# Kernel optimization log

Hardware: AMD Instinct MI355X
Metric: run time of the kernel (lower is better)

Reference implementation:

```python
import jax, jax.numpy as jnp
import numpy as np

B, T, E = 1024, 200, 64
NU, NM, NC = 100000, 1000000, 1000
D_LAU_IN = 8 * E      # 512
D_MLP_IN = 7 * E      # 448
EPS = 1e-5
NEG = -2.0 ** 31


def setup_inputs() -> dict:
    key = jax.random.key(0)
    ks = jax.random.split(key, 32)
    f = lambda k, shape, s=0.05: (jax.random.normal(k, shape, dtype=jnp.float32) * s)
    inp = {
        "uid": jax.random.randint(ks[0], (B,), 0, NU, dtype=jnp.int32),
        "mid": jax.random.randint(ks[1], (B,), 0, NM, dtype=jnp.int32),
        "cat": jax.random.randint(ks[2], (B,), 0, NC, dtype=jnp.int32),
        "historical_mid": jax.random.randint(ks[3], (B, T), 0, NM, dtype=jnp.int32),
        "historical_cat": jax.random.randint(ks[4], (B, T), 0, NC, dtype=jnp.int32),
        "mask": jax.random.randint(ks[5], (B, T), 0, 2, dtype=jnp.int32),
        # embedding tables
        "user_table": f(ks[6], (NU, E), 0.1),
        "mat_table": f(ks[7], (NM, E), 0.1),
        "cat_table": f(ks[8], (NC, E), 0.1),
        # LocalActivationUnit: Linear(512,256)->Sigmoid->Linear(256,128)->Sigmoid->Linear(128,1)
        "lau_w1": f(ks[9], (D_LAU_IN, 256)), "lau_b1": f(ks[10], (256,)),
        "lau_w2": f(ks[11], (256, 128)),     "lau_b2": f(ks[12], (128,)),
        "lau_w3": f(ks[13], (128, 1)),       "lau_b3": f(ks[14], (1,)),
        # MLP: BN(448)->Linear(448,512)->BN->LeakyReLU(0.1)->Linear(512,256)->BN->LeakyReLU->Linear(256,2)
        "bn0_g": jnp.ones((D_MLP_IN,), jnp.float32), "bn0_b": jnp.zeros((D_MLP_IN,), jnp.float32),
        "mlp_w1": f(ks[15], (D_MLP_IN, 512)), "mlp_b1": f(ks[16], (512,)),
        "bn1_g": jnp.ones((512,), jnp.float32), "bn1_b": jnp.zeros((512,), jnp.float32),
        "mlp_w2": f(ks[17], (512, 256)),      "mlp_b2": f(ks[18], (256,)),
        "bn2_g": jnp.ones((256,), jnp.float32), "bn2_b": jnp.zeros((256,), jnp.float32),
        "mlp_w3": f(ks[19], (256, 2)),        "mlp_b3": f(ks[20], (2,)),
    }
    return inp


def _bn(x, g, b):
    # torch BatchNorm1d in training mode: batch mean, biased variance
    mu = jnp.mean(x, axis=0)
    var = jnp.var(x, axis=0)
    return (x - mu) * jax.lax.rsqrt(var + EPS) * g + b


def reference(uid, mid, cat, historical_mid, historical_cat, mask,
              user_table, mat_table, cat_table,
              lau_w1, lau_b1, lau_w2, lau_b2, lau_w3, lau_b3,
              bn0_g, bn0_b, mlp_w1, mlp_b1, bn1_g, bn1_b,
              mlp_w2, mlp_b2, bn2_g, bn2_b, mlp_w3, mlp_b3):
    u = user_table[uid]                                             # [B,E]
    cur = jnp.concatenate([mat_table[mid], cat_table[cat]], axis=1)  # [B,2E]
    hist = jnp.concatenate([mat_table[historical_mid],
                            cat_table[historical_cat]], axis=2)      # [B,T,2E]
    maskf = mask.astype(hist.dtype)                                  # [B,T]

    # Local activation unit
    cur_e = jnp.broadcast_to(cur[:, None, :], hist.shape)            # [B,T,2E]
    comb = jnp.concatenate([cur_e, hist, cur_e - hist, cur_e * hist], axis=2)  # [B,T,8E]
    h = jax.nn.sigmoid(comb @ lau_w1 + lau_b1)
    h = jax.nn.sigmoid(h @ lau_w2 + lau_b2)
    aw = (h @ lau_w3 + lau_b3)[..., 0]                               # [B,T]
    masked = jnp.where(mask == 1, aw, jnp.asarray(NEG, aw.dtype))
    scores = jax.nn.softmax(masked, axis=-1) * maskf                 # [B,T]
    lau = jnp.einsum('bt,bte->be', scores, hist)                     # [B,2E]

    # masked mean of history
    hsum = jnp.einsum('bt,bte->be', maskf, hist)
    hmean = hsum / jnp.sum(maskf, axis=1, keepdims=True)

    x = jnp.concatenate([u, cur, lau, hmean], axis=-1)               # [B,7E]
    x = _bn(x, bn0_g, bn0_b)
    x = jax.nn.leaky_relu(_bn(x @ mlp_w1 + mlp_b1, bn1_g, bn1_b), 0.1)
    x = jax.nn.leaky_relu(_bn(x @ mlp_w2 + mlp_b2, bn2_g, bn2_b), 0.1)
    return x @ mlp_w3 + mlp_b3                                        # [B,2]
```

## Files before the change

kernel.cpp:

```cpp
#include <hip/hip_runtime.h>

#define BB 1024
#define TT 200
#define MROWS (BB*TT)

typedef unsigned short u16;
typedef __attribute__((ext_vector_type(8))) short bf16x8;
typedef __attribute__((ext_vector_type(4))) float f32x4;

__device__ __forceinline__ u16 f2bf(float f) {
  unsigned u = __float_as_uint(f);
  u += 0x7fff + ((u >> 16) & 1);
  return (u16)(u >> 16);
}
__device__ __forceinline__ float bf2f(u16 h) {
  return __uint_as_float(((unsigned)h) << 16);
}

__global__ void prep_weights(const float* __restrict__ w1, const float* __restrict__ w2,
                             u16* __restrict__ WpT, float* __restrict__ Wq,
                             u16* __restrict__ W2T) {
  int i = blockIdx.x * 256 + threadIdx.x;
  if (i < 65536) {
    int n = i >> 8, k = i & 255;
    float v;
    if (k < 128) v = w1[(128 + k) * 256 + n] - w1[(256 + k) * 256 + n];
    else         v = w1[(384 + (k - 128)) * 256 + n];
    WpT[n * 256 + k] = f2bf(v);
  } else if (i < 98304) {
    int j = i - 65536;
    int k = j >> 8, jc = j & 255;
    Wq[j] = w1[k * 256 + jc] + w1[(256 + k) * 256 + jc];
  } else if (i < 131072) {
    int j = i - 98304;
    int n = j >> 8, k = j & 255;
    W2T[j] = f2bf(w2[k * 128 + n]);
  }
}

__global__ __launch_bounds__(256) void prep_batch(
    const int* __restrict__ mid, const int* __restrict__ cat,
    const float* __restrict__ mat_table, const float* __restrict__ cat_table,
    const float* __restrict__ lau_b1, const float* __restrict__ Wq,
    float* __restrict__ cur, float* __restrict__ bias1p) {
  int b = blockIdx.x, tid = threadIdx.x;
  __shared__ float curL[128];
  if (tid < 64)        curL[tid] = mat_table[(long)mid[b] * 64 + tid];
  else if (tid < 128)  curL[tid] = cat_table[(long)cat[b] * 64 + (tid - 64)];
  __syncthreads();
  if (tid < 128) cur[b * 128 + tid] = curL[tid];
  float s = lau_b1[tid];
  for (int k = 0; k < 128; ++k) s += curL[k] * Wq[k * 256 + tid];
  bias1p[b * 256 + tid] = s;
}

__global__ __launch_bounds__(256) void lau_fused(
    const int* __restrict__ hmid, const int* __restrict__ hcat,
    const float* __restrict__ mat_table, const float* __restrict__ cat_table,
    const float* __restrict__ cur, const float* __restrict__ bias1p,
    const u16* __restrict__ WpT, const u16* __restrict__ W2T,
    const float* __restrict__ b2, const float* __restrict__ w3,
    const float* __restrict__ b3,
    u16* __restrict__ Xh, float* __restrict__ AW) {
  __shared__ __align__(16) u16 Al[64 * 264];
  __shared__ __align__(16) u16 Bl[256 * 40];
  __shared__ float awp[4][64];
  int tid = threadIdx.x, wave = tid >> 6, l = tid & 63;
  int q = l >> 4, r16 = l & 15;
  long mBase = (long)blockIdx.x * 64;

  for (int i = tid; i < 2048; i += 256) {
    int r = i >> 5, c4 = i & 31;
    long bt = mBase + r;
    int b = (int)(bt / TT);
    int e0 = c4 * 4;
    float4 hv;
    if (e0 < 64) hv = *(const float4*)(mat_table + (long)hmid[bt] * 64 + e0);
    else         hv = *(const float4*)(cat_table + (long)hcat[bt] * 64 + (e0 - 64));
    float4 cv = *(const float4*)(cur + b * 128 + e0);
    u16 hb[4] = {f2bf(hv.x), f2bf(hv.y), f2bf(hv.z), f2bf(hv.w)};
    u16 pb[4] = {f2bf(hv.x * cv.x), f2bf(hv.y * cv.y), f2bf(hv.z * cv.z), f2bf(hv.w * cv.w)};
    *(ushort4*)(Al + r * 264 + e0)       = *(ushort4*)hb;
    *(ushort4*)(Al + r * 264 + 128 + e0) = *(ushort4*)pb;
    *(ushort4*)(Xh + bt * 128 + e0)      = *(ushort4*)hb;
  }

  f32x4 acc1[4][4] = {};
  for (int ki = 0; ki < 8; ++ki) {
    __syncthreads();
    for (int i = tid; i < 1024; i += 256) {
      int n = i >> 2, c = i & 3;
      *(uint4*)(Bl + n * 40 + c * 8) = *(const uint4*)(WpT + n * 256 + ki * 32 + c * 8);
    }
    __syncthreads();
    bf16x8 a[4], bq[4];
    for (int mt = 0; mt < 4; ++mt)
      a[mt] = *(const bf16x8*)(Al + (mt * 16 + r16) * 264 + ki * 32 + q * 8);
    for (int nt = 0; nt < 4; ++nt)
      bq[nt] = *(const bf16x8*)(Bl + (wave * 64 + nt * 16 + r16) * 40 + q * 8);
    for (int mt = 0; mt < 4; ++mt)
      for (int nt = 0; nt < 4; ++nt)
        acc1[mt][nt] = __builtin_amdgcn_mfma_f32_16x16x32_bf16(a[mt], bq[nt], acc1[mt][nt], 0, 0, 0);
  }
  __syncthreads();
  for (int mt = 0; mt < 4; ++mt)
    for (int r = 0; r < 4; ++r) {
      int row = mt * 16 + q * 4 + r;
      int bidx = (int)((mBase + row) / TT);
      const float* bp = bias1p + (long)bidx * 256;
      for (int nt = 0; nt < 4; ++nt) {
        int col = wave * 64 + nt * 16 + r16;
        float z = acc1[mt][nt][r] + bp[col];
        Al[row * 264 + col] = f2bf(1.f / (1.f + __expf(-z)));
      }
    }
  __syncthreads();

  f32x4 acc2[4][2] = {};
  for (int ki = 0; ki < 8; ++ki) {
    __syncthreads();
    for (int i = tid; i < 512; i += 256) {
      int n = i >> 2, c = i & 3;
      *(uint4*)(Bl + n * 40 + c * 8) = *(const uint4*)(W2T + n * 256 + ki * 32 + c * 8);
    }
    __syncthreads();
    bf16x8 a[4], bq[2];
    for (int mt = 0; mt < 4; ++mt)
      a[mt] = *(const bf16x8*)(Al + (mt * 16 + r16) * 264 + ki * 32 + q * 8);
    for (int nt = 0; nt < 2; ++nt)
      bq[nt] = *(const bf16x8*)(Bl + (wave * 32 + nt * 16 + r16) * 40 + q * 8);
    for (int mt = 0; mt < 4; ++mt)
      for (int nt = 0; nt < 2; ++nt)
        acc2[mt][nt] = __builtin_amdgcn_mfma_f32_16x16x32_bf16(a[mt], bq[nt], acc2[mt][nt], 0, 0, 0);
  }
  float rp[4][4];
  for (int mt = 0; mt < 4; ++mt)
    for (int r = 0; r < 4; ++r) rp[mt][r] = 0.f;
  for (int nt = 0; nt < 2; ++nt) {
    int col = wave * 32 + nt * 16 + r16;
    float b2v = b2[col], w3v = w3[col];
    for (int mt = 0; mt < 4; ++mt)
      for (int r = 0; r < 4; ++r) {
        float z = acc2[mt][nt][r] + b2v;
        rp[mt][r] += w3v / (1.f + __expf(-z));
      }
  }
  for (int off = 1; off < 16; off <<= 1)
    for (int mt = 0; mt < 4; ++mt)
      for (int r = 0; r < 4; ++r)
        rp[mt][r] += __shfl_xor(rp[mt][r], off, 16);
  if (r16 == 0)
    for (int mt = 0; mt < 4; ++mt)
      for (int r = 0; r < 4; ++r)
        awp[wave][mt * 16 + q * 4 + r] = rp[mt][r];
  __syncthreads();
  if (tid < 64)
    AW[mBase + tid] = awp[0][tid] + awp[1][tid] + awp[2][tid] + awp[3][tid] + b3[0];
}

__global__ __launch_bounds__(256) void softmax_pool(
    const float* __restrict__ AW, const int* __restrict__ mask,
    const int* __restrict__ uid, const float* __restrict__ user_table,
    const float* __restrict__ cur, const u16* __restrict__ Xh,
    float* __restrict__ Xmlp) {
  int b = blockIdx.x, tid = threadIdx.x;
  __shared__ float red[256];
  __shared__ float sc[TT], mkf[TT];
  __shared__ float ps[512];
  int mk = 0;
  float masked = -3.0e38f;
  if (tid < TT) {
    mk = mask[b * TT + tid];
    masked = mk ? AW[b * TT + tid] : -2147483648.0f;
  }
  red[tid] = masked; __syncthreads();
  for (int s = 128; s > 0; s >>= 1) { if (tid < s) red[tid] = fmaxf(red[tid], red[tid + s]); __syncthreads(); }
  float mx = red[0]; __syncthreads();
  float ev = (tid < TT) ? __expf(masked - mx) : 0.f;
  red[tid] = ev; __syncthreads();
  for (int s = 128; s > 0; s >>= 1) { if (tid < s) red[tid] += red[tid + s]; __syncthreads(); }
  float denom = red[0]; __syncthreads();
  red[tid] = (tid < TT) ? (float)mk : 0.f; __syncthreads();
  for (int s = 128; s > 0; s >>= 1) { if (tid < s) red[tid] += red[tid + s]; __syncthreads(); }
  float cnt = red[0]; __syncthreads();
  if (tid < TT) { sc[tid] = (ev / denom) * (float)mk; mkf[tid] = (float)mk; }
  __syncthreads();
  int c = tid & 127, p = tid >> 7;
  const u16* xb = Xh + (long)b * TT * 128 + c;
  float sL = 0.f, sH = 0.f;
  for (int t = p; t < TT; t += 2) {
    float hv = bf2f(xb[(long)t * 128]);
    sL += sc[t] * hv;
    sH += mkf[t] * hv;
  }
  ps[tid] = sL; ps[256 + tid] = sH;
  __syncthreads();
  if (tid < 128) {
    float lau  = ps[tid] + ps[tid + 128];
    float hsum = ps[256 + tid] + ps[256 + tid + 128];
    Xmlp[b * 448 + 192 + tid] = lau;
    Xmlp[b * 448 + 320 + tid] = hsum / cnt;
  } else {
    int j = tid - 128;
    Xmlp[b * 448 + 64 + j] = cur[b * 128 + j];
    if (j < 64) Xmlp[b * 448 + j] = user_table[(long)uid[b] * 64 + j];
  }
}

__global__ __launch_bounds__(256) void colstats(const float* __restrict__ X, int cols,
                                                float* __restrict__ psum,
                                                float* __restrict__ psq) {
  int cg = blockIdx.x, rc = blockIdx.y;
  int c = threadIdx.x & 63, ty = threadIdx.x >> 6;
  int col = cg * 64 + c;
  float s = 0.f, ss = 0.f;
  for (int i = 0; i < 16; ++i) {
    int r = rc * 64 + ty + i * 4;
    float v = X[(long)r * cols + col];
    s += v; ss += v * v;
  }
  __shared__ float s1[256], s2[256];
  s1[threadIdx.x] = s; s2[threadIdx.x] = ss;
  __syncthreads();
  if (ty == 0) {
    s  = s1[c] + s1[c + 64] + s1[c + 128] + s1[c + 192];
    ss = s2[c] + s2[c + 64] + s2[c + 128] + s2[c + 192];
    psum[rc * cols + col] = s;
    psq [rc * cols + col] = ss;
  }
}

template <bool LEAKY>
__global__ __launch_bounds__(256) void gemm_bn(
    const float* __restrict__ A, int K,
    const float* __restrict__ psumA, const float* __restrict__ psqA,
    const float* __restrict__ g, const float* __restrict__ bta,
    const float* __restrict__ W, const float* __restrict__ bias, int N,
    float* __restrict__ C, float* __restrict__ psumC, float* __restrict__ psqC) {
  __shared__ float As[16][65], Bs[16][65];
  __shared__ float scK[512], shK[512];
  __shared__ float colS[16][64], colQ[16][64];
  int tid = threadIdx.x;
  for (int j = tid; j < K; j += 256) {
    float s = 0.f, ss = 0.f;
    for (int rc = 0; rc < 16; ++rc) { s += psumA[rc * K + j]; ss += psqA[rc * K + j]; }
    float mu = s * (1.f / 1024.f), var = ss * (1.f / 1024.f) - mu * mu;
    float scv = rsqrtf(var + 1e-5f) * g[j];
    scK[j] = scv; shK[j] = bta[j] - mu * scv;
  }
  __syncthreads();
  int m0 = blockIdx.x * 64, n0 = blockIdx.y * 64;
  int tx = tid & 15, ty = tid >> 4;
  float acc[4][4] = {};
  for (int k0 = 0; k0 < K; k0 += 16) {
    __syncthreads();
    for (int i = tid; i < 1024; i += 256) {
      int m = i >> 4, k = i & 15;
      float v = A[(long)(m0 + m) * K + k0 + k] * scK[k0 + k] + shK[k0 + k];
      if (LEAKY) v = v > 0.f ? v : 0.1f * v;
      As[k][m] = v;
    }
    for (int i = tid; i < 1024; i += 256) {
      int k = i >> 6, n = i & 63;
      Bs[k][n] = W[(long)(k0 + k) * N + n0 + n];
    }
    __syncthreads();
    for (int k = 0; k < 16; ++k) {
      float a[4], bq[4];
      for (int ii = 0; ii < 4; ++ii) a[ii]  = As[k][ty * 4 + ii];
      for (int jj = 0; jj < 4; ++jj) bq[jj] = Bs[k][tx * 4 + jj];
      for (int ii = 0; ii < 4; ++ii)
        for (int jj = 0; jj < 4; ++jj) acc[ii][jj] += a[ii] * bq[jj];
    }
  }
  for (int jj = 0; jj < 4; ++jj) {
    int n = n0 + tx * 4 + jj;
    float bv = bias[n];
    float cs = 0.f, cq = 0.f;
    for (int ii = 0; ii < 4; ++ii) {
      float val = acc[ii][jj] + bv;
      C[(long)(m0 + ty * 4 + ii) * N + n] = val;
      cs += val; cq += val * val;
    }
    colS[ty][tx * 4 + jj] = cs;
    colQ[ty][tx * 4 + jj] = cq;
    __syncthreads();
    if (tid < 64) {
      float s = 0.f, ss = 0.f;
      for (int t = 0; t < 16; ++t) { s += colS[t][tid]; ss += colQ[t][tid]; }
      if ((tid & 3) == jj) {
      }
    }
    __syncthreads();
  }
  for (int jj = 0; jj < 4; ++jj) {
    int n = n0 + tx * 4 + jj;
    float bv = bias[n];
    float cs = 0.f, cq = 0.f;
    for (int ii = 0; ii < 4; ++ii) {
      float val = acc[ii][jj] + bv;
      cs += val; cq += val * val;
    }
    colS[ty][tx * 4 + jj] = cs;
    colQ[ty][tx * 4 + jj] = cq;
    __syncthreads();
    if (tid < 64) {
      float s = 0.f, ss = 0.f;
      for (int t = 0; t < 16; ++t) { s += colS[t][tid]; ss += colQ[t][tid]; }
      if (tid >= jj * 16 && tid < jj * 16 + 16) {  }
      psumC[blockIdx.x * N + n0 + tid] = s;
      psqC [blockIdx.x * N + n0 + tid] = ss;
    }
    __syncthreads();
    break;
  }
}

__global__ __launch_bounds__(256) void final_out(
    const float* __restrict__ y2,
    const float* __restrict__ psum2, const float* __restrict__ psq2,
    const float* __restrict__ g, const float* __restrict__ bta,
    const float* __restrict__ w3, const float* __restrict__ b3,
    float* __restrict__ out) {
  __shared__ float sc2[256], sh2[256];
  __shared__ float p0[256], p1[256];
  int tid = threadIdx.x;
  {
    float s = 0.f, ss = 0.f;
    for (int rc = 0; rc < 16; ++rc) { s += psum2[rc * 256 + tid]; ss += psq2[rc * 256 + tid]; }
    float mu = s * (1.f / 1024.f), var = ss * (1.f / 1024.f) - mu * mu;
    float scv = rsqrtf(var + 1e-5f) * g[tid];
    sc2[tid] = scv; sh2[tid] = bta[tid] - mu * scv;
  }
  __syncthreads();
  int row = blockIdx.x * 64 + (tid >> 2), q = tid & 3;
  const float* yr = y2 + (long)row * 256;
  float a0 = 0.f, a1 = 0.f;
  for (int k = q * 64; k < q * 64 + 64; ++k) {
    float v = yr[k] * sc2[k] + sh2[k];
    v = v > 0.f ? v : 0.1f * v;
    a0 += v * w3[2 * k];
    a1 += v * w3[2 * k + 1];
  }
  p0[tid] = a0; p1[tid] = a1;
  __syncthreads();
  if (q == 0) {
    out[row * 2 + 0] = p0[tid] + p0[tid + 1] + p0[tid + 2] + p0[tid + 3] + b3[0];
    out[row * 2 + 1] = p1[tid] + p1[tid + 1] + p1[tid + 2] + p1[tid + 3] + b3[1];
  }
}


extern "C" void kernel_launch(void* const* d_in, const int* in_sizes, int n_in,
                              void* d_out, int out_size, void* d_ws, size_t ws_size,
                              hipStream_t stream) {
  const int* uid  = (const int*)d_in[0];
  const int* mid  = (const int*)d_in[1];
  const int* cat  = (const int*)d_in[2];
  const int* hmid = (const int*)d_in[3];
  const int* hcat = (const int*)d_in[4];
  const int* mask = (const int*)d_in[5];
  const float* user_table = (const float*)d_in[6];
  const float* mat_table  = (const float*)d_in[7];
  const float* cat_table  = (const float*)d_in[8];
  const float* lau_w1 = (const float*)d_in[9];
  const float* lau_b1 = (const float*)d_in[10];
  const float* lau_w2 = (const float*)d_in[11];
  const float* lau_b2 = (const float*)d_in[12];
  const float* lau_w3 = (const float*)d_in[13];
  const float* lau_b3 = (const float*)d_in[14];
  const float* bn0_g = (const float*)d_in[15];
  const float* bn0_b = (const float*)d_in[16];
  const float* mlp_w1 = (const float*)d_in[17];
  const float* mlp_b1 = (const float*)d_in[18];
  const float* bn1_g = (const float*)d_in[19];
  const float* bn1_b = (const float*)d_in[20];
  const float* mlp_w2 = (const float*)d_in[21];
  const float* mlp_b2 = (const float*)d_in[22];
  const float* bn2_g = (const float*)d_in[23];
  const float* bn2_b = (const float*)d_in[24];
  const float* mlp_w3 = (const float*)d_in[25];
  const float* mlp_b3 = (const float*)d_in[26];
  float* out = (float*)d_out;

  char* w = (char*)d_ws;
  size_t off = 0;
  auto take = [&](size_t bytes) { size_t o = off; off += (bytes + 255) & ~(size_t)255; return o; };
  u16*   Xh     = (u16*)  (w + take((size_t)MROWS * 128 * 2));
  float* AW     = (float*)(w + take((size_t)MROWS * 4));
  float* cur    = (float*)(w + take((size_t)BB * 128 * 4));
  float* bias1p = (float*)(w + take((size_t)BB * 256 * 4));
  float* xmlp   = (float*)(w + take((size_t)BB * 448 * 4));
  float* y1     = (float*)(w + take((size_t)BB * 512 * 4));
  float* y2     = (float*)(w + take((size_t)BB * 256 * 4));
  u16*   WpT    = (u16*)  (w + take(256 * 256 * 2));
  float* Wq     = (float*)(w + take(128 * 256 * 4));
  u16*   W2T    = (u16*)  (w + take(128 * 256 * 2));
  float* psum0  = (float*)(w + take(16 * 448 * 4));
  float* psq0   = (float*)(w + take(16 * 448 * 4));
  float* psum1  = (float*)(w + take(16 * 512 * 4));
  float* psq1   = (float*)(w + take(16 * 512 * 4));
  float* psum2  = (float*)(w + take(16 * 256 * 4));
  float* psq2   = (float*)(w + take(16 * 256 * 4));

  prep_weights<<<512, 256, 0, stream>>>(lau_w1, lau_w2, WpT, Wq, W2T);
  prep_batch<<<BB, 256, 0, stream>>>(mid, cat, mat_table, cat_table, lau_b1, Wq, cur, bias1p);
  lau_fused<<<MROWS / 64, 256, 0, stream>>>(hmid, hcat, mat_table, cat_table, cur, bias1p,
                                            WpT, W2T, lau_b2, lau_w3, lau_b3, Xh, AW);
  softmax_pool<<<BB, 256, 0, stream>>>(AW, mask, uid, user_table, cur, Xh, xmlp);
  {
    dim3 g(448 / 64, 16);
    colstats<<<g, 256, 0, stream>>>(xmlp, 448, psum0, psq0);
  }
  {
    dim3 g(16, 512 / 64);
    gemm_bn<false><<<g, 256, 0, stream>>>(xmlp, 448, psum0, psq0, bn0_g, bn0_b,
                                          mlp_w1, mlp_b1, 512, y1, psum1, psq1);
  }
  {
    dim3 g(16, 256 / 64);
    gemm_bn<true><<<g, 256, 0, stream>>>(y1, 512, psum1, psq1, bn1_g, bn1_b,
                                         mlp_w2, mlp_b2, 256, y2, psum2, psq2);
  }
  final_out<<<16, 256, 0, stream>>>(y2, psum2, psq2, bn2_g, bn2_b, mlp_w3, mlp_b3, out);
}
```

Measured before the change: 779.9 us.

## Read LAU weight fragments directly from global memory and simplify BN-stat epilogue

The fused attention-unit kernel no longer stages weight tiles in shared memory with two barriers per k-step. Each wave now loads its MFMA B fragments straight from the small, cache-resident transposed weight arrays, and the loops are fully unrolled. This removes 32 block-wide barriers and the LDS round trip per tile, at the cost of strided global loads that depend on L1/L2 hit rates. Separately, the MLP GEMM epilogue stops recomputing and re-reducing the column statistics in a redundant second loop and does a single shared-memory reduction.

```diff
diff --git a/kernel.cpp b/kernel.cpp
--- a/kernel.cpp
+++ b/kernel.cpp
@@ -63,7 +63,6 @@
     const float* __restrict__ b3,
     u16* __restrict__ Xh, float* __restrict__ AW) {
   __shared__ __align__(16) u16 Al[64 * 264];
-  __shared__ __align__(16) u16 Bl[256 * 40];
   __shared__ float awp[4][64];
   int tid = threadIdx.x, wave = tid >> 6, l = tid & 63;
   int q = l >> 4, r16 = l & 15;
@@ -84,30 +83,33 @@
     *(ushort4*)(Al + r * 264 + 128 + e0) = *(ushort4*)pb;
     *(ushort4*)(Xh + bt * 128 + e0)      = *(ushort4*)hb;
   }
+  __syncthreads();
 
   f32x4 acc1[4][4] = {};
+  const u16* wp1 = WpT + ((long)(wave * 64 + r16)) * 256 + q * 8;
+  #pragma unroll
   for (int ki = 0; ki < 8; ++ki) {
-    __syncthreads();
-    for (int i = tid; i < 1024; i += 256) {
-      int n = i >> 2, c = i & 3;
-      *(uint4*)(Bl + n * 40 + c * 8) = *(const uint4*)(WpT + n * 256 + ki * 32 + c * 8);
-    }
-    __syncthreads();
-    bf16x8 a[4], bq[4];
+    bf16x8 a[4];
+    #pragma unroll
     for (int mt = 0; mt < 4; ++mt)
       a[mt] = *(const bf16x8*)(Al + (mt * 16 + r16) * 264 + ki * 32 + q * 8);
-    for (int nt = 0; nt < 4; ++nt)
-      bq[nt] = *(const bf16x8*)(Bl + (wave * 64 + nt * 16 + r16) * 40 + q * 8);
-    for (int mt = 0; mt < 4; ++mt)
-      for (int nt = 0; nt < 4; ++nt)
-        acc1[mt][nt] = __builtin_amdgcn_mfma_f32_16x16x32_bf16(a[mt], bq[nt], acc1[mt][nt], 0, 0, 0);
-  }
-  __syncthreads();
+    #pragma unroll
+    for (int nt = 0; nt < 4; ++nt) {
+      bf16x8 bq = *(const bf16x8*)(wp1 + nt * (16 * 256) + ki * 32);
+      #pragma unroll
+      for (int mt = 0; mt < 4; ++mt)
+        acc1[mt][nt] = __builtin_amdgcn_mfma_f32_16x16x32_bf16(a[mt], bq, acc1[mt][nt], 0, 0, 0);
+    }
+  }
+  __syncthreads();
+  #pragma unroll
   for (int mt = 0; mt < 4; ++mt)
+    #pragma unroll
     for (int r = 0; r < 4; ++r) {
       int row = mt * 16 + q * 4 + r;
       int bidx = (int)((mBase + row) / TT);
       const float* bp = bias1p + (long)bidx * 256;
+      #pragma unroll
       for (int nt = 0; nt < 4; ++nt) {
         int col = wave * 64 + nt * 16 + r16;
         float z = acc1[mt][nt][r] + bp[col];
@@ -117,40 +119,49 @@
   __syncthreads();
 
   f32x4 acc2[4][2] = {};
+  const u16* wp2 = W2T + ((long)(wave * 32 + r16)) * 256 + q * 8;
+  #pragma unroll
   for (int ki = 0; ki < 8; ++ki) {
-    __syncthreads();
-    for (int i = tid; i < 512; i += 256) {
-      int n = i >> 2, c = i & 3;
-      *(uint4*)(Bl + n * 40 + c * 8) = *(const uint4*)(W2T + n * 256 + ki * 32 + c * 8);
-    }
-    __syncthreads();
-    bf16x8 a[4], bq[2];
+    bf16x8 a[4];
+    #pragma unroll
     for (int mt = 0; mt < 4; ++mt)
       a[mt] = *(const bf16x8*)(Al + (mt * 16 + r16) * 264 + ki * 32 + q * 8);
-    for (int nt = 0; nt < 2; ++nt)
-      bq[nt] = *(const bf16x8*)(Bl + (wave * 32 + nt * 16 + r16) * 40 + q * 8);
-    for (int mt = 0; mt < 4; ++mt)
-      for (int nt = 0; nt < 2; ++nt)
-        acc2[mt][nt] = __builtin_amdgcn_mfma_f32_16x16x32_bf16(a[mt], bq[nt], acc2[mt][nt], 0, 0, 0);
+    #pragma unroll
+    for (int nt = 0; nt < 2; ++nt) {
+      bf16x8 bq = *(const bf16x8*)(wp2 + nt * (16 * 256) + ki * 32);
+      #pragma unroll
+      for (int mt = 0; mt < 4; ++mt)
+        acc2[mt][nt] = __builtin_amdgcn_mfma_f32_16x16x32_bf16(a[mt], bq, acc2[mt][nt], 0, 0, 0);
+    }
   }
   float rp[4][4];
+  #pragma unroll
   for (int mt = 0; mt < 4; ++mt)
+    #pragma unroll
     for (int r = 0; r < 4; ++r) rp[mt][r] = 0.f;
+  #pragma unroll
   for (int nt = 0; nt < 2; ++nt) {
     int col = wave * 32 + nt * 16 + r16;
     float b2v = b2[col], w3v = w3[col];
+    #pragma unroll
     for (int mt = 0; mt < 4; ++mt)
+      #pragma unroll
       for (int r = 0; r < 4; ++r) {
         float z = acc2[mt][nt][r] + b2v;
         rp[mt][r] += w3v / (1.f + __expf(-z));
       }
   }
+  #pragma unroll
   for (int off = 1; off < 16; off <<= 1)
+    #pragma unroll
     for (int mt = 0; mt < 4; ++mt)
+      #pragma unroll
       for (int r = 0; r < 4; ++r)
         rp[mt][r] += __shfl_xor(rp[mt][r], off, 16);
   if (r16 == 0)
+    #pragma unroll
     for (int mt = 0; mt < 4; ++mt)
+      #pragma unroll
       for (int r = 0; r < 4; ++r)
         awp[wave][mt * 16 + q * 4 + r] = rp[mt][r];
   __syncthreads();
@@ -273,6 +284,7 @@
         for (int jj = 0; jj < 4; ++jj) acc[ii][jj] += a[ii] * bq[jj];
     }
   }
+  float cs4[4], cq4[4];
   for (int jj = 0; jj < 4; ++jj) {
     int n = n0 + tx * 4 + jj;
     float bv = bias[n];
@@ -282,37 +294,19 @@
       C[(long)(m0 + ty * 4 + ii) * N + n] = val;
       cs += val; cq += val * val;
     }
-    colS[ty][tx * 4 + jj] = cs;
-    colQ[ty][tx * 4 + jj] = cq;
-    __syncthreads();
-    if (tid < 64) {
-      float s = 0.f, ss = 0.f;
-      for (int t = 0; t < 16; ++t) { s += colS[t][tid]; ss += colQ[t][tid]; }
-      if ((tid & 3) == jj) {
-      }
-    }
-    __syncthreads();
-  }
+    cs4[jj] = cs; cq4[jj] = cq;
+  }
+  __syncthreads();
   for (int jj = 0; jj < 4; ++jj) {
-    int n = n0 + tx * 4 + jj;
-    float bv = bias[n];
-    float cs = 0.f, cq = 0.f;
-    for (int ii = 0; ii < 4; ++ii) {
-      float val = acc[ii][jj] + bv;
-      cs += val; cq += val * val;
-    }
-    colS[ty][tx * 4 + jj] = cs;
-    colQ[ty][tx * 4 + jj] = cq;
-    __syncthreads();
-    if (tid < 64) {
-      float s = 0.f, ss = 0.f;
-      for (int t = 0; t < 16; ++t) { s += colS[t][tid]; ss += colQ[t][tid]; }
-      if (tid >= jj * 16 && tid < jj * 16 + 16) {  }
-      psumC[blockIdx.x * N + n0 + tid] = s;
-      psqC [blockIdx.x * N + n0 + tid] = ss;
-    }
-    __syncthreads();
-    break;
+    colS[ty][tx * 4 + jj] = cs4[jj];
+    colQ[ty][tx * 4 + jj] = cq4[jj];
+  }
+  __syncthreads();
+  if (tid < 64) {
+    float s = 0.f, ss = 0.f;
+    for (int t = 0; t < 16; ++t) { s += colS[t][tid]; ss += colQ[t][tid]; }
+    psumC[blockIdx.x * N + n0 + tid] = s;
+    psqC [blockIdx.x * N + n0 + tid] = ss;
   }
 }
 
```

Result: faster. 748.1 us (-4.1%).
